# Kernel optimization log

Measured on AMD Instinct MI355X. Metric: run time of the kernel, lower is better.

The kernel has to match this reference:

```python
import jax, jax.numpy as jnp
import numpy as np

N_NODES = 50000
N_EDGES = 600000
N_PAIRS = 200000
D_IN, D_HID = 128, 256


def _sage_conv(x, src, dst, W_l, b_l, W_r, num_nodes):
    # PyG SAGEConv('mean'): out = mean_agg(x_j) @ W_l + b_l + x @ W_r
    msgs = x[src]                                              # [E, d] gather
    agg = jax.ops.segment_sum(msgs, dst, num_segments=num_nodes)
    deg = jax.ops.segment_sum(jnp.ones((src.shape[0],), x.dtype), dst,
                              num_segments=num_nodes)
    agg = agg / jnp.maximum(deg, 1.0)[:, None]                 # mean, safe for deg=0
    return agg @ W_l + b_l + x @ W_r


def setup_inputs() -> dict:
    key = jax.random.key(0)
    ks = jax.random.split(key, 8)
    s = lambda d: 1.0 / np.sqrt(d)
    return {
        "features": jax.random.normal(ks[0], (N_NODES, D_IN), jnp.float32),
        "edge_index": jax.random.randint(ks[1], (2, N_EDGES), 0, N_NODES, jnp.int64),
        "mask": jax.random.randint(ks[2], (N_PAIRS, 2), 0, N_NODES, jnp.int64),
        "W1l": jax.random.normal(ks[3], (D_IN, D_HID), jnp.float32) * s(D_IN),
        "b1l": jnp.zeros((D_HID,), jnp.float32),
        "W1r": jax.random.normal(ks[4], (D_IN, D_HID), jnp.float32) * s(D_IN),
        "W2l": jax.random.normal(ks[5], (D_HID, D_IN), jnp.float32) * s(D_HID),
        "b2l": jnp.zeros((D_IN,), jnp.float32),
        "W2r": jax.random.normal(ks[6], (D_HID, D_IN), jnp.float32) * s(D_HID),
        "Wlin": jax.random.normal(ks[7], (2 * D_IN, 1), jnp.float32) * s(2 * D_IN),
        "blin": jnp.zeros((1,), jnp.float32),
    }


def reference(features, edge_index, mask, W1l, b1l, W1r, W2l, b2l, W2r, Wlin, blin):
    n = features.shape[0]
    src, dst = edge_index[0], edge_index[1]
    h = _sage_conv(features, src, dst, W1l, b1l, W1r, n)       # [N, 256]
    h = jax.nn.relu(h)                                         # dropout p=0 -> identity
    h = _sage_conv(h, src, dst, W2l, b2l, W2r, n)              # [N, 128]
    m = mask.T                                                 # [2, P]
    p1 = jax.lax.stop_gradient(h[m[0]])                        # detach in original
    p2 = jax.lax.stop_gradient(h[m[1]])
    pair = jnp.concatenate((p1, p2), axis=1)                   # [P, 256]
    return jax.nn.sigmoid(pair @ Wlin + blin)                  # [P, 1]
```

## Files before the change

kernel.cpp:

```cpp
#include <hip/hip_runtime.h>
#include <math.h>

#define NN 50000
#define NE 600000
#define NP 200000
#define NB_SCAN 49

typedef unsigned int uint;
typedef unsigned short ushort;
typedef __attribute__((ext_vector_type(8))) short bf16x8;
typedef __attribute__((ext_vector_type(4))) float f32x4;

__device__ __forceinline__ ushort f2bf(float f) {
    uint u = __float_as_uint(f);
    uint r = (u + 0x7FFFu + ((u >> 16) & 1u)) >> 16;
    return (ushort)r;
}
__device__ __forceinline__ float bf2f(uint lo16) {
    return __uint_as_float(lo16 << 16);
}

__device__ __forceinline__ int wave_iscan(int v, int lane) {
#pragma unroll
    for (int off = 1; off < 64; off <<= 1) {
        int t = __shfl_up(v, off, 64);
        if (lane >= off) v += t;
    }
    return v;
}

template <int K, int N>
__device__ __forceinline__ void prepB_one(int idx, const float* __restrict__ Wt,
                                          const float* __restrict__ Wb,
                                          ushort* __restrict__ Bp) {
    int lane = idx & 63;
    int nt = (idx >> 6) % (N / 16);
    int ct = idx / (64 * (N / 16));
    int n = nt * 16 + (lane & 15);
    int kb = ct * 32 + (lane >> 4) * 8;
#pragma unroll
    for (int j = 0; j < 8; j++) {
        int k = kb + j;
        float w = (k < K / 2) ? Wt[(size_t)k * N + n] : Wb[(size_t)(k - K / 2) * N + n];
        Bp[(size_t)idx * 8 + j] = f2bf(w);
    }
}

#define T_PREP (NN * 32)
#define T_DEG  (T_PREP + NE)
#define T_B1   (T_DEG + 8192)
#define T_PQ   (T_B1 + 1024)
#define T_CAB  (T_PQ + 2)
__global__ void k_pre(const float* __restrict__ x, uint* __restrict__ xb,
                      const int* __restrict__ dst, int* __restrict__ deg,
                      const float* __restrict__ W1l, const float* __restrict__ W1r,
                      ushort* __restrict__ Bp1,
                      const float* __restrict__ W2l, const float* __restrict__ W2r,
                      const float* __restrict__ Wlin, const float* __restrict__ b2l,
                      float* __restrict__ pq, float* __restrict__ cab) {
    int t = blockIdx.x * 256 + threadIdx.x;
    if (t < T_PREP) {
        int n = t >> 5, c4 = t & 31;
        float4 v = *(const float4*)(x + (size_t)n * 128 + c4 * 4);
        uint2 o;
        o.x = (uint)f2bf(v.x) | ((uint)f2bf(v.y) << 16);
        o.y = (uint)f2bf(v.z) | ((uint)f2bf(v.w) << 16);
        *(uint2*)(xb + (size_t)n * 64 + c4 * 2) = o;
    } else if (t < T_DEG) {
        atomicAdd(deg + dst[t - T_PREP], 1);
    } else if (t < T_B1) {
        prepB_one<256, 256>(t - T_DEG, W1l, W1r, Bp1);
    } else if (t < T_PQ) {
        int idx = t - T_B1;
        int vec = idx >> 8;
        int k = idx & 255;
        const float* W = (vec < 2) ? W2l : W2r;
        const float* wl = Wlin + (vec & 1) * 128;
        float s = 0.f;
#pragma unroll 4
        for (int j = 0; j < 128; j++) s += W[(size_t)k * 128 + j] * wl[j];
        pq[idx] = s;
    } else if (t < T_CAB) {
        int i = t - T_PQ;
        float s = 0.f;
        for (int j = 0; j < 128; j++) s += b2l[j] * Wlin[i * 128 + j];
        cab[i] = s;
    }
}

__global__ __launch_bounds__(1024) void k_scanfill(const int* __restrict__ deg,
                                                   int* __restrict__ bsum,
                                                   int* __restrict__ flags,
                                                   int* __restrict__ rowptr,
                                                   int* __restrict__ cursor,
                                                   const int* __restrict__ src,
                                                   const int* __restrict__ dst,
                                                   int* __restrict__ ssrc) {
    int tid = threadIdx.x;
    int i = blockIdx.x * 1024 + tid;
    int lane = tid & 63, wid = tid >> 6;
    int v = (i < NN) ? deg[i] : 0;
    int incl = wave_iscan(v, lane);
    __shared__ int wt[16];
    __shared__ int sboff;
    if (lane == 63) wt[wid] = incl;
    __syncthreads();
    if (tid < 16) {
        int w = wt[tid];
#pragma unroll
        for (int off = 1; off < 16; off <<= 1) {
            int t = __shfl_up(w, off, 64);
            if (tid >= off) w += t;
        }
        wt[tid] = w;
    }
    __syncthreads();
    int base = (wid > 0) ? wt[wid - 1] : 0;
    int excl_local = incl - v + base;
    if (tid == 0)
        __hip_atomic_store(&bsum[blockIdx.x], wt[15], __ATOMIC_RELEASE,
                           __HIP_MEMORY_SCOPE_AGENT);
    __syncthreads();
    if (tid == 0) {
        __hip_atomic_fetch_add(&flags[0], 1, __ATOMIC_ACQ_REL, __HIP_MEMORY_SCOPE_AGENT);
        while (__hip_atomic_load(&flags[0], __ATOMIC_ACQUIRE,
                                 __HIP_MEMORY_SCOPE_AGENT) < NB_SCAN) {}
    }
    __syncthreads();
    if (tid < 64) {
        int b = (tid < NB_SCAN && tid < (int)blockIdx.x)
                    ? __hip_atomic_load(&bsum[tid], __ATOMIC_ACQUIRE,
                                        __HIP_MEMORY_SCOPE_AGENT)
                    : 0;
#pragma unroll
        for (int off = 1; off < 64; off <<= 1) b += __shfl_xor(b, off, 64);
        if (tid == 0) sboff = b;
    }
    __syncthreads();
    int boff = sboff;
    if (i < NN) {
        int rv = excl_local + boff;
        rowptr[i] = rv;
        __hip_atomic_store(&cursor[i], rv, __ATOMIC_RELAXED, __HIP_MEMORY_SCOPE_AGENT);
    }
    if (i == 0) rowptr[NN] = NE;
    __syncthreads();
    if (tid == 0) {
        __hip_atomic_fetch_add(&flags[1], 1, __ATOMIC_ACQ_REL, __HIP_MEMORY_SCOPE_AGENT);
        while (__hip_atomic_load(&flags[1], __ATOMIC_ACQUIRE,
                                 __HIP_MEMORY_SCOPE_AGENT) < NB_SCAN) {}
    }
    __syncthreads();
    const int STRIDE = NB_SCAN * 4096;
    for (int e0 = blockIdx.x * 4096 + tid * 4; e0 < NE; e0 += STRIDE) {
        int4 d4 = *(const int4*)(dst + e0);
        int4 s4 = *(const int4*)(src + e0);
        int p0 = __hip_atomic_fetch_add(&cursor[d4.x], 1, __ATOMIC_RELAXED,
                                        __HIP_MEMORY_SCOPE_AGENT);
        int p1 = __hip_atomic_fetch_add(&cursor[d4.y], 1, __ATOMIC_RELAXED,
                                        __HIP_MEMORY_SCOPE_AGENT);
        int p2 = __hip_atomic_fetch_add(&cursor[d4.z], 1, __ATOMIC_RELAXED,
                                        __HIP_MEMORY_SCOPE_AGENT);
        int p3 = __hip_atomic_fetch_add(&cursor[d4.w], 1, __ATOMIC_RELAXED,
                                        __HIP_MEMORY_SCOPE_AGENT);
        ssrc[p0] = s4.x;
        ssrc[p1] = s4.y;
        ssrc[p2] = s4.z;
        ssrc[p3] = s4.w;
    }
}

#define LDSROW 264
__global__ __launch_bounds__(256) void k_agg_gemm(const uint* __restrict__ xb,
                                                  const ushort* __restrict__ Bp,
                                                  const int* __restrict__ rowptr,
                                                  const int* __restrict__ ssrc,
                                                  const float* __restrict__ bias,
                                                  const float* __restrict__ pq,
                                                  float2* __restrict__ g2,
                                                  float2* __restrict__ u2) {
    __shared__ ushort At[32][LDSROW];
    __shared__ float red[4][4][32];
    const int NTW = 4;
    int tid = threadIdx.x;
    int wave = tid >> 6, lane = tid & 63;
    int g = lane >> 4, s = lane & 15;
    int mbase = blockIdx.x * 32;

#pragma unroll
    for (int it = 0; it < 2; it++) {
        int idx = it * 256 + tid;
        int row = idx >> 4, c = idx & 15;
        int node = mbase + row;
        if (node >= NN) node = NN - 1;
        uint4 v = *(const uint4*)(xb + (size_t)node * 64 + c * 4);
        *(uint4*)(&At[row][128 + c * 8]) = v;
    }

    for (int q = 0; q < 8; q++) {
        int tr = wave * 8 + q;
        int n = mbase + tr;
        if (n < NN) {
            int r0 = rowptr[n], r1 = rowptr[n + 1];
            float a0[8] = {0.f, 0.f, 0.f, 0.f, 0.f, 0.f, 0.f, 0.f};
            float a1[8] = {0.f, 0.f, 0.f, 0.f, 0.f, 0.f, 0.f, 0.f};
            int e = r0;
            for (; e + 8 <= r1; e += 8) {
                int sA = ssrc[e + g];
                int sB = ssrc[e + 4 + g];
                uint4 vA = *(const uint4*)(xb + (size_t)sA * 64 + s * 4);
                uint4 vB = *(const uint4*)(xb + (size_t)sB * 64 + s * 4);
                a0[0] += bf2f(vA.x & 0xffffu); a0[1] += bf2f(vA.x >> 16);
                a0[2] += bf2f(vA.y & 0xffffu); a0[3] += bf2f(vA.y >> 16);
                a0[4] += bf2f(vA.z & 0xffffu); a0[5] += bf2f(vA.z >> 16);
                a0[6] += bf2f(vA.w & 0xffffu); a0[7] += bf2f(vA.w >> 16);
                a1[0] += bf2f(vB.x & 0xffffu); a1[1] += bf2f(vB.x >> 16);
                a1[2] += bf2f(vB.y & 0xffffu); a1[3] += bf2f(vB.y >> 16);
                a1[4] += bf2f(vB.z & 0xffffu); a1[5] += bf2f(vB.z >> 16);
                a1[6] += bf2f(vB.w & 0xffffu); a1[7] += bf2f(vB.w >> 16);
            }
            if (e + 4 <= r1) {
                int sA = ssrc[e + g];
                uint4 vA = *(const uint4*)(xb + (size_t)sA * 64 + s * 4);
                a0[0] += bf2f(vA.x & 0xffffu); a0[1] += bf2f(vA.x >> 16);
                a0[2] += bf2f(vA.y & 0xffffu); a0[3] += bf2f(vA.y >> 16);
                a0[4] += bf2f(vA.z & 0xffffu); a0[5] += bf2f(vA.z >> 16);
                a0[6] += bf2f(vA.w & 0xffffu); a0[7] += bf2f(vA.w >> 16);
                e += 4;
            }
            int rem = r1 - e;
            if (g < rem) {
                int sB = ssrc[e + g];
                uint4 vB = *(const uint4*)(xb + (size_t)sB * 64 + s * 4);
                a1[0] += bf2f(vB.x & 0xffffu); a1[1] += bf2f(vB.x >> 16);
                a1[2] += bf2f(vB.y & 0xffffu); a1[3] += bf2f(vB.y >> 16);
                a1[4] += bf2f(vB.z & 0xffffu); a1[5] += bf2f(vB.z >> 16);
                a1[6] += bf2f(vB.w & 0xffffu); a1[7] += bf2f(vB.w >> 16);
            }
            float ax[8];
#pragma unroll
            for (int j = 0; j < 8; j++) ax[j] = a0[j] + a1[j];
#pragma unroll
            for (int j = 0; j < 8; j++) {
                ax[j] += __shfl_xor(ax[j], 16, 64);
                ax[j] += __shfl_xor(ax[j], 32, 64);
            }
            if (g == 0) {
                float sc = 1.0f / fmaxf((float)(r1 - r0), 1.0f);
                uint4 o;
                o.x = (uint)f2bf(ax[0] * sc) | ((uint)f2bf(ax[1] * sc) << 16);
                o.y = (uint)f2bf(ax[2] * sc) | ((uint)f2bf(ax[3] * sc) << 16);
                o.z = (uint)f2bf(ax[4] * sc) | ((uint)f2bf(ax[5] * sc) << 16);
                o.w = (uint)f2bf(ax[6] * sc) | ((uint)f2bf(ax[7] * sc) << 16);
                *(uint4*)(&At[tr][s * 8]) = o;
            }
        } else if (g == 0) {
            *(uint4*)(&At[tr][s * 8]) = make_uint4(0, 0, 0, 0);
        }
    }
    __syncthreads();

    int quad = lane >> 4, l15 = lane & 15;
    f32x4 acc0[NTW], acc1[NTW];
#pragma unroll
    for (int i = 0; i < NTW; i++) {
        acc0[i] = (f32x4){0.f, 0.f, 0.f, 0.f};
        acc1[i] = (f32x4){0.f, 0.f, 0.f, 0.f};
    }
    const bf16x8* bp = (const bf16x8*)Bp;
#pragma unroll
    for (int ct = 0; ct < 8; ct++) {
        bf16x8 a0 = *(const bf16x8*)(&At[l15][ct * 32 + quad * 8]);
        bf16x8 a1 = *(const bf16x8*)(&At[16 + l15][ct * 32 + quad * 8]);
#pragma unroll
        for (int ntl = 0; ntl < NTW; ntl++) {
            int nt = wave * NTW + ntl;
            bf16x8 b = bp[(ct * 16 + nt) * 64 + lane];
            acc0[ntl] = __builtin_amdgcn_mfma_f32_16x16x32_bf16(a0, b, acc0[ntl], 0, 0, 0);
            acc1[ntl] = __builtin_amdgcn_mfma_f32_16x16x32_bf16(a1, b, acc1[ntl], 0, 0, 0);
        }
    }
    float pga[2][4] = {{0,0,0,0},{0,0,0,0}}, pgb[2][4] = {{0,0,0,0},{0,0,0,0}};
    float pua[2][4] = {{0,0,0,0},{0,0,0,0}}, pub[2][4] = {{0,0,0,0},{0,0,0,0}};
#pragma unroll
    for (int ntl = 0; ntl < NTW; ntl++) {
        int col = (wave * NTW + ntl) * 16 + l15;
        float bv = bias[col];
        float wpa = pq[col], wpb = pq[256 + col];
        float wqa = pq[512 + col], wqb = pq[768 + col];
#pragma unroll
        for (int reg = 0; reg < 4; reg++) {
            float v0 = acc0[ntl][reg] + bv;  v0 = v0 > 0.f ? v0 : 0.f;
            float v1 = acc1[ntl][reg] + bv;  v1 = v1 > 0.f ? v1 : 0.f;
            pga[0][reg] += v0 * wpa;  pgb[0][reg] += v0 * wpb;
            pua[0][reg] += v0 * wqa;  pub[0][reg] += v0 * wqb;
            pga[1][reg] += v1 * wpa;  pgb[1][reg] += v1 * wpb;
            pua[1][reg] += v1 * wqa;  pub[1][reg] += v1 * wqb;
        }
    }
#pragma unroll
    for (int off = 1; off < 16; off <<= 1) {
#pragma unroll
        for (int rt = 0; rt < 2; rt++) {
#pragma unroll
            for (int reg = 0; reg < 4; reg++) {
                pga[rt][reg] += __shfl_xor(pga[rt][reg], off, 64);
                pgb[rt][reg] += __shfl_xor(pgb[rt][reg], off, 64);
                pua[rt][reg] += __shfl_xor(pua[rt][reg], off, 64);
                pub[rt][reg] += __shfl_xor(pub[rt][reg], off, 64);
            }
        }
    }
    if (l15 == 0) {
#pragma unroll
        for (int rt = 0; rt < 2; rt++) {
#pragma unroll
            for (int reg = 0; reg < 4; reg++) {
                int row = rt * 16 + quad * 4 + reg;
                red[0][wave][row] = pga[rt][reg];
                red[1][wave][row] = pgb[rt][reg];
                red[2][wave][row] = pua[rt][reg];
                red[3][wave][row] = pub[rt][reg];
            }
        }
    }
    __syncthreads();
    if (threadIdx.x < 32) {
        int row = threadIdx.x;
        int m = mbase + row;
        if (m < NN) {
            float ga = (red[0][0][row] + red[0][1][row]) + (red[0][2][row] + red[0][3][row]);
            float gb = (red[1][0][row] + red[1][1][row]) + (red[1][2][row] + red[1][3][row]);
            float ua = (red[2][0][row] + red[2][1][row]) + (red[2][2][row] + red[2][3][row]);
            float ub = (red[3][0][row] + red[3][1][row]) + (red[3][2][row] + red[3][3][row]);
            g2[m] = make_float2(ga, gb);
            u2[m] = make_float2(ua, ub);
        }
    }
}

__global__ void k_sagg(const float2* __restrict__ g2, const float2* __restrict__ u2,
                       const int* __restrict__ rowptr, const int* __restrict__ ssrc,
                       const float* __restrict__ cab,
                       float* __restrict__ sa, float* __restrict__ sb) {
    int n = blockIdx.x * 256 + threadIdx.x;
    if (n >= NN) return;
    int r0 = rowptr[n], r1 = rowptr[n + 1];
    float a0 = 0.f, b0 = 0.f, a1 = 0.f, b1 = 0.f;
    float a2 = 0.f, b2 = 0.f, a3 = 0.f, b3 = 0.f;
    int e = r0;
    for (; e + 4 <= r1; e += 4) {
        float2 v0 = g2[ssrc[e]];
        float2 v1 = g2[ssrc[e + 1]];
        float2 v2 = g2[ssrc[e + 2]];
        float2 v3 = g2[ssrc[e + 3]];
        a0 += v0.x; b0 += v0.y;
        a1 += v1.x; b1 += v1.y;
        a2 += v2.x; b2 += v2.y;
        a3 += v3.x; b3 += v3.y;
    }
    for (; e < r1; e++) {
        float2 v = g2[ssrc[e]];
        a0 += v.x; b0 += v.y;
    }
    float sc = 1.0f / fmaxf((float)(r1 - r0), 1.0f);
    float2 u = u2[n];
    sa[n] = ((a0 + a1) + (a2 + a3)) * sc + u.x + cab[0];
    sb[n] = ((b0 + b1) + (b2 + b3)) * sc + u.y + cab[1];
}

__global__ void k_pairs(const float* __restrict__ sa, const float* __restrict__ sb,
                        const int* __restrict__ mask, const float* __restrict__ blin,
                        float* __restrict__ out) {
    int p = blockIdx.x * 256 + threadIdx.x;
    if (p >= NP) return;
    int2 m = ((const int2*)mask)[p];
    float v = sa[m.x] + sb[m.y] + blin[0];
    out[p] = 1.0f / (1.0f + __expf(-v));
}

extern "C" void kernel_launch(void* const* d_in, const int* in_sizes, int n_in,
                              void* d_out, int out_size, void* d_ws, size_t ws_size,
                              hipStream_t stream) {
    const float* x    = (const float*)d_in[0];
    const int*   ei   = (const int*)  d_in[1];
    const int*   mask = (const int*)  d_in[2];
    const float* W1l  = (const float*)d_in[3];
    const float* b1l  = (const float*)d_in[4];
    const float* W1r  = (const float*)d_in[5];
    const float* W2l  = (const float*)d_in[6];
    const float* b2l  = (const float*)d_in[7];
    const float* W2r  = (const float*)d_in[8];
    const float* Wlin = (const float*)d_in[9];
    const float* blin = (const float*)d_in[10];
    float* out = (float*)d_out;

    const int* src = ei;
    const int* dst = ei + NE;

    char* ws = (char*)d_ws;
    int*    deg    = (int*)(ws);
    int*    flags  = (int*)(ws + 0xF0000);
    int*    rowptr = (int*)(ws + (size_t)1 * (1 << 20));
    int*    cursor = (int*)(ws + (size_t)2 * (1 << 20));
    int*    ssrc   = (int*)(ws + (size_t)3 * (1 << 20));
    int*    bsum   = (int*)(ws + (size_t)6 * (1 << 20));
    ushort* Bp1    = (ushort*)(ws + (size_t)8 * (1 << 20));
    float*  pq     = (float*)(ws + (size_t)9 * (1 << 20));
    float*  cab    = (float*)(ws + (size_t)9 * (1 << 20) + 65536);
    float*  sa     = (float*)(ws + (size_t)10 * (1 << 20));
    float*  sb     = (float*)(ws + (size_t)11 * (1 << 20));
    float2* g2     = (float2*)(ws + (size_t)12 * (1 << 20));
    float2* u2     = (float2*)(ws + (size_t)13 * (1 << 20));
    uint*   xb     = (uint*)(ws + (size_t)14 * (1 << 20));

    hipMemsetAsync(ws, 0, (size_t)1 << 20, stream);

    k_pre     <<<(T_CAB + 255) / 256, 256, 0, stream>>>(x, xb, dst, deg,
                                                        W1l, W1r, Bp1,
                                                        W2l, W2r, Wlin, b2l, pq, cab);
    k_scanfill<<<NB_SCAN, 1024, 0, stream>>>(deg, bsum, flags, rowptr, cursor,
                                             src, dst, ssrc);
    k_agg_gemm<<<(NN + 31) / 32, 256, 0, stream>>>(xb, Bp1, rowptr, ssrc, b1l,
                                                   pq, g2, u2);
    k_sagg    <<<(NN + 255) / 256, 256, 0, stream>>>(g2, u2, rowptr, ssrc, cab, sa, sb);
    k_pairs   <<<(NP + 255) / 256, 256, 0, stream>>>(sa, sb, mask, blin, out);
}
```

Baseline: 244.3 us.

## Split fused neighbor aggregation and GEMM into separate kernels

```diff
diff --git a/kernel.cpp b/kernel.cpp
--- a/kernel.cpp
+++ b/kernel.cpp
@@ -170,97 +170,84 @@
     }
 }
 
-#define LDSROW 264
-__global__ __launch_bounds__(256) void k_agg_gemm(const uint* __restrict__ xb,
-                                                  const ushort* __restrict__ Bp,
-                                                  const int* __restrict__ rowptr,
-                                                  const int* __restrict__ ssrc,
-                                                  const float* __restrict__ bias,
-                                                  const float* __restrict__ pq,
-                                                  float2* __restrict__ g2,
-                                                  float2* __restrict__ u2) {
-    __shared__ ushort At[32][LDSROW];
-    __shared__ float red[4][4][32];
+__global__ void k_agg1(const uint* __restrict__ xb, uint* __restrict__ aggb,
+                       const int* __restrict__ rowptr, const int* __restrict__ ssrc) {
+    int t = blockIdx.x * 256 + threadIdx.x;
+    int n = t >> 6;
+    if (n >= NN) return;
+    int lane = t & 63;
+    int g = lane >> 4;
+    int s = lane & 15;
+    int r0 = rowptr[n], r1 = rowptr[n + 1];
+    float a0[8] = {0.f, 0.f, 0.f, 0.f, 0.f, 0.f, 0.f, 0.f};
+    float a1[8] = {0.f, 0.f, 0.f, 0.f, 0.f, 0.f, 0.f, 0.f};
+    int e = r0;
+    for (; e + 8 <= r1; e += 8) {
+        int sA = ssrc[e + g];
+        int sB = ssrc[e + 4 + g];
+        uint4 vA = *(const uint4*)(xb + (size_t)sA * 64 + s * 4);
+        uint4 vB = *(const uint4*)(xb + (size_t)sB * 64 + s * 4);
+        a0[0] += bf2f(vA.x & 0xffffu); a0[1] += bf2f(vA.x >> 16);
+        a0[2] += bf2f(vA.y & 0xffffu); a0[3] += bf2f(vA.y >> 16);
+        a0[4] += bf2f(vA.z & 0xffffu); a0[5] += bf2f(vA.z >> 16);
+        a0[6] += bf2f(vA.w & 0xffffu); a0[7] += bf2f(vA.w >> 16);
+        a1[0] += bf2f(vB.x & 0xffffu); a1[1] += bf2f(vB.x >> 16);
+        a1[2] += bf2f(vB.y & 0xffffu); a1[3] += bf2f(vB.y >> 16);
+        a1[4] += bf2f(vB.z & 0xffffu); a1[5] += bf2f(vB.z >> 16);
+        a1[6] += bf2f(vB.w & 0xffffu); a1[7] += bf2f(vB.w >> 16);
+    }
+    if (e + 4 <= r1) {
+        int sA = ssrc[e + g];
+        uint4 vA = *(const uint4*)(xb + (size_t)sA * 64 + s * 4);
+        a0[0] += bf2f(vA.x & 0xffffu); a0[1] += bf2f(vA.x >> 16);
+        a0[2] += bf2f(vA.y & 0xffffu); a0[3] += bf2f(vA.y >> 16);
+        a0[4] += bf2f(vA.z & 0xffffu); a0[5] += bf2f(vA.z >> 16);
+        a0[6] += bf2f(vA.w & 0xffffu); a0[7] += bf2f(vA.w >> 16);
+        e += 4;
+    }
+    int rem = r1 - e;
+    if (g < rem) {
+        int sB = ssrc[e + g];
+        uint4 vB = *(const uint4*)(xb + (size_t)sB * 64 + s * 4);
+        a1[0] += bf2f(vB.x & 0xffffu); a1[1] += bf2f(vB.x >> 16);
+        a1[2] += bf2f(vB.y & 0xffffu); a1[3] += bf2f(vB.y >> 16);
+        a1[4] += bf2f(vB.z & 0xffffu); a1[5] += bf2f(vB.z >> 16);
+        a1[6] += bf2f(vB.w & 0xffffu); a1[7] += bf2f(vB.w >> 16);
+    }
+    float ax[8];
+#pragma unroll
+    for (int j = 0; j < 8; j++) ax[j] = a0[j] + a1[j];
+#pragma unroll
+    for (int j = 0; j < 8; j++) {
+        ax[j] += __shfl_xor(ax[j], 16, 64);
+        ax[j] += __shfl_xor(ax[j], 32, 64);
+    }
+    if (g == 0) {
+        float sc = 1.0f / fmaxf((float)(r1 - r0), 1.0f);
+        uint4 o;
+        o.x = (uint)f2bf(ax[0] * sc) | ((uint)f2bf(ax[1] * sc) << 16);
+        o.y = (uint)f2bf(ax[2] * sc) | ((uint)f2bf(ax[3] * sc) << 16);
+        o.z = (uint)f2bf(ax[4] * sc) | ((uint)f2bf(ax[5] * sc) << 16);
+        o.w = (uint)f2bf(ax[6] * sc) | ((uint)f2bf(ax[7] * sc) << 16);
+        *(uint4*)(aggb + (size_t)n * 64 + s * 4) = o;
+    }
+}
+
+__global__ __launch_bounds__(256) void k_gemm1(const ushort* __restrict__ agg,
+                                               const ushort* __restrict__ xbu,
+                                               const ushort* __restrict__ Bp,
+                                               const float* __restrict__ bias,
+                                               const float* __restrict__ pq,
+                                               float2* __restrict__ g2,
+                                               float2* __restrict__ u2) {
     const int NTW = 4;
-    int tid = threadIdx.x;
-    int wave = tid >> 6, lane = tid & 63;
-    int g = lane >> 4, s = lane & 15;
+    int wave = threadIdx.x >> 6;
+    int lane = threadIdx.x & 63;
+    int quad = lane >> 4;
+    int l15 = lane & 15;
     int mbase = blockIdx.x * 32;
-
-#pragma unroll
-    for (int it = 0; it < 2; it++) {
-        int idx = it * 256 + tid;
-        int row = idx >> 4, c = idx & 15;
-        int node = mbase + row;
-        if (node >= NN) node = NN - 1;
-        uint4 v = *(const uint4*)(xb + (size_t)node * 64 + c * 4);
-        *(uint4*)(&At[row][128 + c * 8]) = v;
-    }
-
-    for (int q = 0; q < 8; q++) {
-        int tr = wave * 8 + q;
-        int n = mbase + tr;
-        if (n < NN) {
-            int r0 = rowptr[n], r1 = rowptr[n + 1];
-            float a0[8] = {0.f, 0.f, 0.f, 0.f, 0.f, 0.f, 0.f, 0.f};
-            float a1[8] = {0.f, 0.f, 0.f, 0.f, 0.f, 0.f, 0.f, 0.f};
-            int e = r0;
-            for (; e + 8 <= r1; e += 8) {
-                int sA = ssrc[e + g];
-                int sB = ssrc[e + 4 + g];
-                uint4 vA = *(const uint4*)(xb + (size_t)sA * 64 + s * 4);
-                uint4 vB = *(const uint4*)(xb + (size_t)sB * 64 + s * 4);
-                a0[0] += bf2f(vA.x & 0xffffu); a0[1] += bf2f(vA.x >> 16);
-                a0[2] += bf2f(vA.y & 0xffffu); a0[3] += bf2f(vA.y >> 16);
-                a0[4] += bf2f(vA.z & 0xffffu); a0[5] += bf2f(vA.z >> 16);
-                a0[6] += bf2f(vA.w & 0xffffu); a0[7] += bf2f(vA.w >> 16);
-                a1[0] += bf2f(vB.x & 0xffffu); a1[1] += bf2f(vB.x >> 16);
-                a1[2] += bf2f(vB.y & 0xffffu); a1[3] += bf2f(vB.y >> 16);
-                a1[4] += bf2f(vB.z & 0xffffu); a1[5] += bf2f(vB.z >> 16);
-                a1[6] += bf2f(vB.w & 0xffffu); a1[7] += bf2f(vB.w >> 16);
-            }
-            if (e + 4 <= r1) {
-                int sA = ssrc[e + g];
-                uint4 vA = *(const uint4*)(xb + (size_t)sA * 64 + s * 4);
-                a0[0] += bf2f(vA.x & 0xffffu); a0[1] += bf2f(vA.x >> 16);
-                a0[2] += bf2f(vA.y & 0xffffu); a0[3] += bf2f(vA.y >> 16);
-                a0[4] += bf2f(vA.z & 0xffffu); a0[5] += bf2f(vA.z >> 16);
-                a0[6] += bf2f(vA.w & 0xffffu); a0[7] += bf2f(vA.w >> 16);
-                e += 4;
-            }
-            int rem = r1 - e;
-            if (g < rem) {
-                int sB = ssrc[e + g];
-                uint4 vB = *(const uint4*)(xb + (size_t)sB * 64 + s * 4);
-                a1[0] += bf2f(vB.x & 0xffffu); a1[1] += bf2f(vB.x >> 16);
-                a1[2] += bf2f(vB.y & 0xffffu); a1[3] += bf2f(vB.y >> 16);
-                a1[4] += bf2f(vB.z & 0xffffu); a1[5] += bf2f(vB.z >> 16);
-                a1[6] += bf2f(vB.w & 0xffffu); a1[7] += bf2f(vB.w >> 16);
-            }
-            float ax[8];
-#pragma unroll
-            for (int j = 0; j < 8; j++) ax[j] = a0[j] + a1[j];
-#pragma unroll
-            for (int j = 0; j < 8; j++) {
-                ax[j] += __shfl_xor(ax[j], 16, 64);
-                ax[j] += __shfl_xor(ax[j], 32, 64);
-            }
-            if (g == 0) {
-                float sc = 1.0f / fmaxf((float)(r1 - r0), 1.0f);
-                uint4 o;
-                o.x = (uint)f2bf(ax[0] * sc) | ((uint)f2bf(ax[1] * sc) << 16);
-                o.y = (uint)f2bf(ax[2] * sc) | ((uint)f2bf(ax[3] * sc) << 16);
-                o.z = (uint)f2bf(ax[4] * sc) | ((uint)f2bf(ax[5] * sc) << 16);
-                o.w = (uint)f2bf(ax[6] * sc) | ((uint)f2bf(ax[7] * sc) << 16);
-                *(uint4*)(&At[tr][s * 8]) = o;
-            }
-        } else if (g == 0) {
-            *(uint4*)(&At[tr][s * 8]) = make_uint4(0, 0, 0, 0);
-        }
-    }
-    __syncthreads();
-
-    int quad = lane >> 4, l15 = lane & 15;
+    int r0 = mbase + l15;       if (r0 >= NN) r0 = NN - 1;
+    int r1 = mbase + 16 + l15;  if (r1 >= NN) r1 = NN - 1;
     f32x4 acc0[NTW], acc1[NTW];
 #pragma unroll
     for (int i = 0; i < NTW; i++) {
@@ -270,8 +257,10 @@
     const bf16x8* bp = (const bf16x8*)Bp;
 #pragma unroll
     for (int ct = 0; ct < 8; ct++) {
-        bf16x8 a0 = *(const bf16x8*)(&At[l15][ct * 32 + quad * 8]);
-        bf16x8 a1 = *(const bf16x8*)(&At[16 + l15][ct * 32 + quad * 8]);
+        const ushort* Asrc = (ct < 4) ? agg : xbu;
+        int kc = (ct & 3) * 32 + quad * 8;
+        bf16x8 a0 = *(const bf16x8*)(Asrc + (size_t)r0 * 128 + kc);
+        bf16x8 a1 = *(const bf16x8*)(Asrc + (size_t)r1 * 128 + kc);
 #pragma unroll
         for (int ntl = 0; ntl < NTW; ntl++) {
             int nt = wave * NTW + ntl;
@@ -311,6 +300,7 @@
             }
         }
     }
+    __shared__ float red[4][4][32];
     if (l15 == 0) {
 #pragma unroll
         for (int rt = 0; rt < 2; rt++) {
@@ -413,6 +403,7 @@
     float2* g2     = (float2*)(ws + (size_t)12 * (1 << 20));
     float2* u2     = (float2*)(ws + (size_t)13 * (1 << 20));
     uint*   xb     = (uint*)(ws + (size_t)14 * (1 << 20));
+    uint*   aggb   = (uint*)(ws + (size_t)28 * (1 << 20));
 
     hipMemsetAsync(ws, 0, (size_t)1 << 20, stream);
 
@@ -421,7 +412,9 @@
                                                         W2l, W2r, Wlin, b2l, pq, cab);
     k_scanfill<<<NB_SCAN, 1024, 0, stream>>>(deg, bsum, flags, rowptr, cursor,
                                              src, dst, ssrc);
-    k_agg_gemm<<<(NN + 31) / 32, 256, 0, stream>>>(xb, Bp1, rowptr, ssrc, b1l,
+    k_agg1    <<<NN / 4, 256, 0, stream>>>(xb, aggb, rowptr, ssrc);
+    k_gemm1   <<<(NN + 31) / 32, 256, 0, stream>>>((const ushort*)aggb,
+                                                   (const ushort*)xb, Bp1, b1l,
                                                    pq, g2, u2);
     k_sagg    <<<(NN + 255) / 256, 256, 0, stream>>>(g2, u2, rowptr, ssrc, cab, sa, sb);
     k_pairs   <<<(NP + 255) / 256, 256, 0, stream>>>(sa, sb, mask, blin, out);
```

New measurement: 228.1 us. 1.07x faster.
